# Kernel tuning notes

Measured on AMD Instinct MI355X. Metric: run time of the kernel, lower is better.

The kernel has to match this reference:

```python
import jax, jax.numpy as jnp
import numpy as np

SPATIAL_SHAPES = ((100, 100), (50, 50), (25, 25), (13, 13))
B, C, NH, NL, NP, DFF = 4, 256, 8, 4, 4, 1024
HD = C // NH
L = sum(h * w for h, w in SPATIAL_SHAPES)  # 13294


def _xavier(key, shape):
    s = (6.0 / (shape[0] + shape[1])) ** 0.5
    return jax.random.uniform(key, shape, jnp.float32, -s, s)


def setup_inputs():
    key = jax.random.key(0)
    ks = jax.random.split(key, 12)
    ss = jnp.array(SPATIAL_SHAPES, jnp.int32)
    lsi = jnp.concatenate([jnp.zeros((1,), jnp.int32), jnp.cumsum(ss[:, 0] * ss[:, 1])[:-1].astype(jnp.int32)])
    return {
        "query": jax.random.normal(ks[0], (B, L, C), jnp.float32),
        "query_pos": jax.random.normal(ks[1], (B, L, C), jnp.float32),
        "reference_points": jax.random.uniform(ks[2], (B, L, NL, 2), jnp.float32),
        "spatial_shapes": ss,
        "level_start_index": lsi,
        "v_W": _xavier(ks[3], (C, C)), "v_b": jnp.zeros((C,), jnp.float32),
        "off_W": 0.01 * jax.random.normal(ks[4], (C, NH * NL * NP * 2), jnp.float32),
        "off_b": 0.1 * jax.random.normal(ks[5], (NH * NL * NP * 2,), jnp.float32),
        "aw_W": 0.01 * jax.random.normal(ks[6], (C, NH * NL * NP), jnp.float32),
        "aw_b": jnp.zeros((NH * NL * NP,), jnp.float32),
        "out_W": _xavier(ks[7], (C, C)), "out_b": jnp.zeros((C,), jnp.float32),
        "ln1_g": jnp.ones((C,), jnp.float32), "ln1_b": jnp.zeros((C,), jnp.float32),
        "lin1_W": _xavier(ks[8], (C, DFF)), "lin1_b": jnp.zeros((DFF,), jnp.float32),
        "lin2_W": _xavier(ks[9], (DFF, C)), "lin2_b": jnp.zeros((C,), jnp.float32),
        "ln2_g": jnp.ones((C,), jnp.float32), "ln2_b": jnp.zeros((C,), jnp.float32),
    }


def _layer_norm(x, g, b):
    mu = x.mean(-1, keepdims=True)
    var = ((x - mu) ** 2).mean(-1, keepdims=True)
    return (x - mu) * jax.lax.rsqrt(var + 1e-5) * g + b


def _msda(q, value, reference_points, v_W, v_b, off_W, off_b, aw_W, aw_b, out_W, out_b):
    # value projection, split heads -> [B, NH, L, HD]
    v = (value @ v_W + v_b).reshape(B, L, NH, HD).transpose(0, 2, 1, 3)
    off = (q @ off_W + off_b).reshape(B, L, NH, NL, NP, 2)
    aw = jax.nn.softmax((q @ aw_W + aw_b).reshape(B, L, NH, NL * NP), axis=-1)
    aw = aw.reshape(B, L, NH, NL, NP).transpose(0, 2, 1, 3, 4)  # [B,NH,L,NL,NP]
    # offset normalizer is (W, H) per level, matching (x, y) coords
    norm = jnp.array([[w, h] for h, w in SPATIAL_SHAPES], q.dtype)
    loc = reference_points[:, :, None, :, None, :] + off / norm[None, None, None, :, None, :]
    loc = loc.transpose(0, 2, 1, 3, 4, 5)  # [B,NH,L,NL,NP,2]
    acc = jnp.zeros((B, NH, L, HD), q.dtype)
    start = 0
    for l, (H_, W_) in enumerate(SPATIAL_SHAPES):
        v_l = jax.lax.dynamic_slice_in_dim(v, start, H_ * W_, axis=2)  # [B,NH,HW,HD]
        # grid_sample(align_corners=False): pixel = loc*size - 0.5
        x = loc[:, :, :, l, :, 0] * W_ - 0.5  # [B,NH,L,NP]
        y = loc[:, :, :, l, :, 1] * H_ - 0.5
        x0 = jnp.floor(x); y0 = jnp.floor(y)
        lx = x - x0; ly = y - y0
        x0i = x0.astype(jnp.int32); y0i = y0.astype(jnp.int32)

        def corner(yi, xi, w):
            valid = (yi >= 0) & (yi < H_) & (xi >= 0) & (xi < W_)  # zero padding
            idx = jnp.clip(yi, 0, H_ - 1) * W_ + jnp.clip(xi, 0, W_ - 1)
            g = jnp.take_along_axis(v_l, idx.reshape(B, NH, L * NP, 1), axis=2)
            g = g.reshape(B, NH, L, NP, HD)
            return g * (w * valid)[..., None]

        s = (corner(y0i, x0i, (1 - ly) * (1 - lx))
             + corner(y0i, x0i + 1, (1 - ly) * lx)
             + corner(y0i + 1, x0i, ly * (1 - lx))
             + corner(y0i + 1, x0i + 1, ly * lx))  # [B,NH,L,NP,HD]
        acc = acc + (s * aw[:, :, :, l, :, None]).sum(3)
        start += H_ * W_
    out = acc.transpose(0, 2, 1, 3).reshape(B, L, C)
    return out @ out_W + out_b


def _forward(query, query_pos, reference_points, v_W, v_b, off_W, off_b, aw_W, aw_b,
             out_W, out_b, ln1_g, ln1_b, lin1_W, lin1_b, lin2_W, lin2_b, ln2_g, ln2_b):
    q = query + query_pos
    src2 = _msda(q, query, reference_points, v_W, v_b, off_W, off_b, aw_W, aw_b, out_W, out_b)
    x = _layer_norm(query + src2, ln1_g, ln1_b)
    ffn = jax.nn.relu(x @ lin1_W + lin1_b) @ lin2_W + lin2_b
    return _layer_norm(x + ffn, ln2_g, ln2_b)


def reference(query, query_pos, reference_points, spatial_shapes, level_start_index,
              v_W, v_b, off_W, off_b, aw_W, aw_b, out_W, out_b,
              ln1_g, ln1_b, lin1_W, lin1_b, lin2_W, lin2_b, ln2_g, ln2_b):
    # spatial_shapes / level_start_index are consistent with the static SPATIAL_SHAPES
    # constant (shapes must be static for reshapes under jit).
    return _forward(query, query_pos, reference_points, v_W, v_b, off_W, off_b, aw_W, aw_b,
                    out_W, out_b, ln1_g, ln1_b, lin1_W, lin1_b, lin2_W, lin2_b, ln2_g, ln2_b)
```

## Files before the change

### kernel.cpp

```cpp
#include <hip/hip_runtime.h>
#include <hip/hip_bf16.h>
#include <cstddef>

constexpr int Ll   = 13294;
constexpr int NROW = 4 * Ll;
constexpr int MP   = 53248;

typedef __bf16       bf8v __attribute__((ext_vector_type(8)));
typedef float        f4v  __attribute__((ext_vector_type(4)));
typedef unsigned int u4v  __attribute__((ext_vector_type(4)));

template<bool RELU, bool OUTF, bool OUTB>
__global__ __launch_bounds__(256)
void gemm_mfma(const __hip_bfloat16* __restrict__ A, const __hip_bfloat16* __restrict__ Bt,
               const float* __restrict__ bias, const float* __restrict__ bias2,
               float* __restrict__ Cf, __hip_bfloat16* __restrict__ Cb,
               int M, int N, int K)
{
    __shared__ __hip_bfloat16 As[128 * 32];
    __shared__ __hip_bfloat16 Bs[128 * 32];
    const int tid  = threadIdx.x;
    const int wid  = tid >> 6;
    const int lane = tid & 63;
    const int m0 = blockIdx.y * 128;
    const int n0 = blockIdx.x * 128;
    const int wm = wid >> 1, wn = wid & 1;
    const int fr = lane & 15, fq = lane >> 4;
    const int sr = lane >> 2;
    const int sc = (lane & 3) * 8;

    f4v acc[4][4] = {};

    for (int k0 = 0; k0 < K; k0 += 32) {
        #pragma unroll
        for (int i = 0; i < 2; ++i) {
            const int s = wid * 2 + i;
            const __hip_bfloat16* sa = A  + (size_t)(m0 + s * 16 + sr) * K + k0 + sc;
            const __hip_bfloat16* sb = Bt + (size_t)(n0 + s * 16 + sr) * K + k0 + sc;
            __builtin_amdgcn_global_load_lds(
                (const __attribute__((address_space(1))) void*)sa,
                (__attribute__((address_space(3))) void*)&As[s * 512], 16, 0, 0);
            __builtin_amdgcn_global_load_lds(
                (const __attribute__((address_space(1))) void*)sb,
                (__attribute__((address_space(3))) void*)&Bs[s * 512], 16, 0, 0);
        }
        __syncthreads();

        bf8v a[4], b[4];
        #pragma unroll
        for (int r = 0; r < 4; ++r) {
            a[r] = __builtin_bit_cast(bf8v, *(const u4v*)&As[(wm * 64 + r * 16 + fr) * 32 + fq * 8]);
            b[r] = __builtin_bit_cast(bf8v, *(const u4v*)&Bs[(wn * 64 + r * 16 + fr) * 32 + fq * 8]);
        }
        #pragma unroll
        for (int nr = 0; nr < 4; ++nr)
            #pragma unroll
            for (int mr = 0; mr < 4; ++mr)
                acc[nr][mr] = __builtin_amdgcn_mfma_f32_16x16x32_bf16(b[nr], a[mr], acc[nr][mr], 0, 0, 0);
        __syncthreads();
    }

    #pragma unroll
    for (int nr = 0; nr < 4; ++nr) {
        const int colbase = n0 + wn * 64 + nr * 16 + fq * 4;
        const float* bp = (bias2 != nullptr && colbase >= 256) ? (bias2 - 256) : bias;
        const float4 b4 = *(const float4*)&bp[colbase];
        #pragma unroll
        for (int mr = 0; mr < 4; ++mr) {
            const int row = m0 + wm * 64 + mr * 16 + fr;
            f4v v = acc[nr][mr];
            v[0] += b4.x; v[1] += b4.y; v[2] += b4.z; v[3] += b4.w;
            if (RELU) {
                v[0] = fmaxf(v[0], 0.f); v[1] = fmaxf(v[1], 0.f);
                v[2] = fmaxf(v[2], 0.f); v[3] = fmaxf(v[3], 0.f);
            }
            if (OUTF)
                *(float4*)&Cf[(size_t)row * N + colbase] = make_float4(v[0], v[1], v[2], v[3]);
            if (OUTB) {
                union { ushort4 u; __hip_bfloat16 h[4]; } pk;
                pk.h[0] = __float2bfloat16(v[0]); pk.h[1] = __float2bfloat16(v[1]);
                pk.h[2] = __float2bfloat16(v[2]); pk.h[3] = __float2bfloat16(v[3]);
                *(ushort4*)&Cb[(size_t)row * N + colbase] = pk.u;
            }
        }
    }
}

template<bool STOREB, bool RESB>
__global__ __launch_bounds__(256)
void gemm_ln(const __hip_bfloat16* __restrict__ A, const __hip_bfloat16* __restrict__ Bt,
             const float* __restrict__ bias,
             const float* __restrict__ resF, const __hip_bfloat16* __restrict__ resB,
             int Mres,
             const float* __restrict__ g, const float* __restrict__ be,
             float* __restrict__ outF, int MstoreF,
             __hip_bfloat16* __restrict__ outB,
             int K)
{
    __shared__ __hip_bfloat16 As[64 * 32];
    __shared__ __hip_bfloat16 Bs[256 * 32];
    __shared__ float red[2][64][2];
    const int tid  = threadIdx.x;
    const int wid  = tid >> 6;
    const int lane = tid & 63;
    const int m0 = blockIdx.x * 64;
    const int wm = wid >> 1, wn = wid & 1;
    const int fr = lane & 15, fq = lane >> 4;
    const int sr = lane >> 2;
    const int sc = (lane & 3) * 8;

    f4v acc[8][2] = {};

    for (int k0 = 0; k0 < K; k0 += 32) {
        {
            const __hip_bfloat16* sa = A + (size_t)(m0 + wid * 16 + sr) * K + k0 + sc;
            __builtin_amdgcn_global_load_lds(
                (const __attribute__((address_space(1))) void*)sa,
                (__attribute__((address_space(3))) void*)&As[wid * 512], 16, 0, 0);
        }
        #pragma unroll
        for (int i = 0; i < 4; ++i) {
            const int s = wid * 4 + i;
            const __hip_bfloat16* sb = Bt + (size_t)(s * 16 + sr) * K + k0 + sc;
            __builtin_amdgcn_global_load_lds(
                (const __attribute__((address_space(1))) void*)sb,
                (__attribute__((address_space(3))) void*)&Bs[s * 512], 16, 0, 0);
        }
        __syncthreads();

        bf8v a[2], b[8];
        #pragma unroll
        for (int r = 0; r < 2; ++r)
            a[r] = __builtin_bit_cast(bf8v, *(const u4v*)&As[(wm * 32 + r * 16 + fr) * 32 + fq * 8]);
        #pragma unroll
        for (int r = 0; r < 8; ++r)
            b[r] = __builtin_bit_cast(bf8v, *(const u4v*)&Bs[(wn * 128 + r * 16 + fr) * 32 + fq * 8]);
        #pragma unroll
        for (int nr = 0; nr < 8; ++nr)
            #pragma unroll
            for (int mr = 0; mr < 2; ++mr)
                acc[nr][mr] = __builtin_amdgcn_mfma_f32_16x16x32_bf16(b[nr], a[mr], acc[nr][mr], 0, 0, 0);
        __syncthreads();
    }

    float s2[2] = {}, q2[2] = {};
    #pragma unroll
    for (int nr = 0; nr < 8; ++nr) {
        const int colbase = wn * 128 + nr * 16 + fq * 4;
        const float4 b4 = *(const float4*)&bias[colbase];
        #pragma unroll
        for (int mr = 0; mr < 2; ++mr) {
            const int row = m0 + wm * 32 + mr * 16 + fr;
            f4v x = acc[nr][mr];
            x[0] += b4.x; x[1] += b4.y; x[2] += b4.z; x[3] += b4.w;
            if (RESB) {
                const ushort4 r4 = *(const ushort4*)&resB[(size_t)row * 256 + colbase];
                x[0] += __builtin_bit_cast(float, (unsigned)r4.x << 16);
                x[1] += __builtin_bit_cast(float, (unsigned)r4.y << 16);
                x[2] += __builtin_bit_cast(float, (unsigned)r4.z << 16);
                x[3] += __builtin_bit_cast(float, (unsigned)r4.w << 16);
            } else if (row < Mres) {
                const float4 r4 = *(const float4*)&resF[(size_t)row * 256 + colbase];
                x[0] += r4.x; x[1] += r4.y; x[2] += r4.z; x[3] += r4.w;
            }
            acc[nr][mr] = x;
            s2[mr] += x[0] + x[1] + x[2] + x[3];
            q2[mr] += x[0]*x[0] + x[1]*x[1] + x[2]*x[2] + x[3]*x[3];
        }
    }
    #pragma unroll
    for (int mr = 0; mr < 2; ++mr) {
        s2[mr] += __shfl_xor(s2[mr], 16, 64);
        q2[mr] += __shfl_xor(q2[mr], 16, 64);
        s2[mr] += __shfl_xor(s2[mr], 32, 64);
        q2[mr] += __shfl_xor(q2[mr], 32, 64);
    }
    if (fq == 0) {
        #pragma unroll
        for (int mr = 0; mr < 2; ++mr) {
            red[wn][wm * 32 + mr * 16 + fr][0] = s2[mr];
            red[wn][wm * 32 + mr * 16 + fr][1] = q2[mr];
        }
    }
    __syncthreads();
    float mean[2], rinv[2];
    #pragma unroll
    for (int mr = 0; mr < 2; ++mr) {
        const int r = wm * 32 + mr * 16 + fr;
        const float ss = red[0][r][0] + red[1][r][0];
        const float qq = red[0][r][1] + red[1][r][1];
        mean[mr] = ss * (1.f / 256.f);
        const float var = qq * (1.f / 256.f) - mean[mr] * mean[mr];
        rinv[mr] = rsqrtf(var + 1e-5f);
    }
    #pragma unroll
    for (int nr = 0; nr < 8; ++nr) {
        const int colbase = wn * 128 + nr * 16 + fq * 4;
        const float4 g4 = *(const float4*)&g[colbase];
        const float4 e4 = *(const float4*)&be[colbase];
        #pragma unroll
        for (int mr = 0; mr < 2; ++mr) {
            const int row = m0 + wm * 32 + mr * 16 + fr;
            const f4v x = acc[nr][mr];
            float y0 = (x[0] - mean[mr]) * rinv[mr] * g4.x + e4.x;
            float y1 = (x[1] - mean[mr]) * rinv[mr] * g4.y + e4.y;
            float y2 = (x[2] - mean[mr]) * rinv[mr] * g4.z + e4.z;
            float y3 = (x[3] - mean[mr]) * rinv[mr] * g4.w + e4.w;
            if (row < MstoreF)
                *(float4*)&outF[(size_t)row * 256 + colbase] = make_float4(y0, y1, y2, y3);
            if (STOREB) {
                union { ushort4 u; __hip_bfloat16 h[4]; } pk;
                pk.h[0] = __float2bfloat16(y0); pk.h[1] = __float2bfloat16(y1);
                pk.h[2] = __float2bfloat16(y2); pk.h[3] = __float2bfloat16(y3);
                *(ushort4*)&outB[(size_t)row * 256 + colbase] = pk.u;
            }
        }
    }
}

__global__ __launch_bounds__(256)
void prep_weights(const float* __restrict__ vW, const float* __restrict__ offW,
                  const float* __restrict__ awW, const float* __restrict__ outW,
                  const float* __restrict__ w1, const float* __restrict__ w2,
                  __hip_bfloat16* __restrict__ vWt, __hip_bfloat16* __restrict__ catWt,
                  __hip_bfloat16* __restrict__ outWt, __hip_bfloat16* __restrict__ w1t,
                  __hip_bfloat16* __restrict__ w2t)
{
    int i = blockIdx.x * 256 + threadIdx.x;
    if (i < 65536) { const int n = i >> 8, k = i & 255;
        vWt[i] = __float2bfloat16(vW[(size_t)k * 256 + n]); return; }
    i -= 65536;
    if (i < 98304) { const int n = i >> 8, k = i & 255;
        catWt[i] = __float2bfloat16(n < 256 ? offW[(size_t)k * 256 + n]
                                            : awW[(size_t)k * 128 + n - 256]); return; }
    i -= 98304;
    if (i < 65536) { const int n = i >> 8, k = i & 255;
        outWt[i] = __float2bfloat16(outW[(size_t)k * 256 + n]); return; }
    i -= 65536;
    if (i < 262144) { const int n = i >> 8, k = i & 255;
        w1t[i] = __float2bfloat16(w1[(size_t)k * 1024 + n]); return; }
    i -= 262144;
    { const int n = i >> 10, k = i & 1023;
        w2t[i] = __float2bfloat16(w2[(size_t)k * 256 + n]); }
}

__global__ __launch_bounds__(256)
void cvt_both(const float* __restrict__ q, const float* __restrict__ qp,
              __hip_bfloat16* __restrict__ qb, __hip_bfloat16* __restrict__ qpb)
{
    const int i   = blockIdx.x * 256 + threadIdx.x;
    const int row = i >> 5;
    union { u4v u; __hip_bfloat16 h[8]; } p1, p2;
    if (row >= NROW) {
        u4v z = {0u, 0u, 0u, 0u};
        p1.u = z; p2.u = z;
    } else {
        const size_t e = (size_t)i * 8;
        float4 x0 = *(const float4*)&q[e];
        float4 x1 = *(const float4*)&q[e + 4];
        float4 y0 = *(const float4*)&qp[e];
        float4 y1 = *(const float4*)&qp[e + 4];
        p1.h[0] = __float2bfloat16(x0.x); p1.h[1] = __float2bfloat16(x0.y);
        p1.h[2] = __float2bfloat16(x0.z); p1.h[3] = __float2bfloat16(x0.w);
        p1.h[4] = __float2bfloat16(x1.x); p1.h[5] = __float2bfloat16(x1.y);
        p1.h[6] = __float2bfloat16(x1.z); p1.h[7] = __float2bfloat16(x1.w);
        p2.h[0] = __float2bfloat16(x0.x + y0.x); p2.h[1] = __float2bfloat16(x0.y + y0.y);
        p2.h[2] = __float2bfloat16(x0.z + y0.z); p2.h[3] = __float2bfloat16(x0.w + y0.w);
        p2.h[4] = __float2bfloat16(x1.x + y1.x); p2.h[5] = __float2bfloat16(x1.y + y1.y);
        p2.h[6] = __float2bfloat16(x1.z + y1.z); p2.h[7] = __float2bfloat16(x1.w + y1.w);
    }
    *(u4v*)&qb[(size_t)i * 8]  = p1.u;
    *(u4v*)&qpb[(size_t)i * 8] = p2.u;
}

__device__ __forceinline__ float blo(unsigned u) { return __builtin_bit_cast(float, u << 16); }
__device__ __forceinline__ float bhi(unsigned u) { return __builtin_bit_cast(float, u & 0xffff0000u); }

__global__ __launch_bounds__(256)
void msda_sample3(const __hip_bfloat16* __restrict__ v, const float* __restrict__ cat,
                  const float* __restrict__ refp, __hip_bfloat16* __restrict__ accO)
{
    __shared__ int   sIdx[1024][4];
    __shared__ float sW[1024][4];
    const int row0 = blockIdx.x * 8;
    const int tid  = threadIdx.x;

    #pragma unroll
    for (int it = 0; it < 4; ++it) {
        const int item = it * 256 + tid;
        const int p = item & 15, h = (item >> 4) & 7, r = item >> 7;
        const int row = row0 + r;
        const int lvl = p >> 2;
        const float logit = cat[(size_t)row * 384 + 256 + h * 16 + p];
        float mx = logit;
        #pragma unroll
        for (int o = 1; o < 16; o <<= 1) mx = fmaxf(mx, __shfl_xor(mx, o, 64));
        const float e = __expf(logit - mx);
        float s = e;
        #pragma unroll
        for (int o = 1; o < 16; o <<= 1) s += __shfl_xor(s, o, 64);
        const float aw = e / s;

        const int Hs[4] = {100, 50, 25, 13};
        const int Ss[4] = {0, 10000, 12500, 13125};
        const int   Wl = Hs[lvl];
        const float Wf = (float)Wl;
        const float ox = cat[(size_t)row * 384 + h * 32 + p * 2 + 0];
        const float oy = cat[(size_t)row * 384 + h * 32 + p * 2 + 1];
        const float rx = refp[(size_t)row * 8 + lvl * 2 + 0];
        const float ry = refp[(size_t)row * 8 + lvl * 2 + 1];
        const float x = (rx + ox / Wf) * Wf - 0.5f;
        const float y = (ry + oy / Wf) * Wf - 0.5f;
        const float x0f = floorf(x), y0f = floorf(y);
        const float lx = x - x0f, ly = y - y0f;
        const int x0 = (int)x0f, y0 = (int)y0f;
        const int b = row / Ll;
        const int vbase = b * Ll + Ss[lvl];
        int ixr[4]; float wr[4];
        #pragma unroll
        for (int c = 0; c < 4; ++c) {
            const int cy = c >> 1, cx = c & 1;
            const int yi = y0 + cy, xi = x0 + cx;
            const bool ok = (yi >= 0) & (yi < Wl) & (xi >= 0) & (xi < Wl);
            const int yc = min(max(yi, 0), Wl - 1);
            const int xc = min(max(xi, 0), Wl - 1);
            const float wt = (cy ? ly : 1.f - ly) * (cx ? lx : 1.f - lx);
            ixr[c] = (vbase + yc * Wl + xc) * 512;
            wr[c]  = ok ? aw * wt : 0.f;
        }
        const int item2 = (item & ~15) | ((item & 15) ^ h);
        *(int4*)&sIdx[item2][0] = make_int4(ixr[0], ixr[1], ixr[2], ixr[3]);
        *(float4*)&sW[item2][0] = make_float4(wr[0], wr[1], wr[2], wr[3]);
    }
    __syncthreads();

    const int r   = tid >> 5;
    const int h   = (tid >> 2) & 7;
    const int oct = tid & 3;
    const int row = row0 + r;
    const char* vB = (const char*)v + (h * 32 + oct * 8) * 2;
    const int ibase = r * 128 + h * 16;
    float acc[8] = {};
    #pragma unroll
    for (int i = 0; i < 16; ++i) {
        const int idx = ibase + (i ^ h);
        const int4   ix = *(const int4*)&sIdx[idx][0];
        const float4 wv = *(const float4*)&sW[idx][0];
        u4v u0 = *(const u4v*)(vB + (unsigned)ix.x);
        u4v u1 = *(const u4v*)(vB + (unsigned)ix.y);
        u4v u2 = *(const u4v*)(vB + (unsigned)ix.z);
        u4v u3 = *(const u4v*)(vB + (unsigned)ix.w);
        #pragma unroll
        for (int q = 0; q < 4; ++q) {
            acc[2*q]   = fmaf(wv.x, blo(u0[q]), acc[2*q]);
            acc[2*q+1] = fmaf(wv.x, bhi(u0[q]), acc[2*q+1]);
            acc[2*q]   = fmaf(wv.y, blo(u1[q]), acc[2*q]);
            acc[2*q+1] = fmaf(wv.y, bhi(u1[q]), acc[2*q+1]);
            acc[2*q]   = fmaf(wv.z, blo(u2[q]), acc[2*q]);
            acc[2*q+1] = fmaf(wv.z, bhi(u2[q]), acc[2*q+1]);
            acc[2*q]   = fmaf(wv.w, blo(u3[q]), acc[2*q]);
            acc[2*q+1] = fmaf(wv.w, bhi(u3[q]), acc[2*q+1]);
        }
    }
    union { u4v u; __hip_bfloat16 hh[8]; } pk;
    #pragma unroll
    for (int q = 0; q < 8; ++q) pk.hh[q] = __float2bfloat16(acc[q]);
    *(u4v*)&accO[(size_t)row * 256 + h * 32 + oct * 8] = pk.u;
}

extern "C" void kernel_launch(void* const* d_in, const int* in_sizes, int n_in,
                              void* d_out, int out_size, void* d_ws, size_t ws_size,
                              hipStream_t stream)
{
    (void)in_sizes; (void)n_in; (void)out_size; (void)ws_size;
    const float* query = (const float*)d_in[0];
    const float* qpos  = (const float*)d_in[1];
    const float* refp  = (const float*)d_in[2];
    const float* v_W   = (const float*)d_in[5];
    const float* v_b   = (const float*)d_in[6];
    const float* off_W = (const float*)d_in[7];
    const float* off_b = (const float*)d_in[8];
    const float* aw_W  = (const float*)d_in[9];
    const float* aw_b  = (const float*)d_in[10];
    const float* out_W = (const float*)d_in[11];
    const float* out_b = (const float*)d_in[12];
    const float* ln1g  = (const float*)d_in[13];
    const float* ln1b  = (const float*)d_in[14];
    const float* w1    = (const float*)d_in[15];
    const float* b1    = (const float*)d_in[16];
    const float* w2    = (const float*)d_in[17];
    const float* b2    = (const float*)d_in[18];
    const float* ln2g  = (const float*)d_in[19];
    const float* ln2b  = (const float*)d_in[20];
    float* out = (float*)d_out;

    char* ws = (char*)d_ws;
    constexpr size_t CATF_B = (size_t)MP * 384 * 4;
    constexpr size_t HALF_B = (size_t)MP * 256 * 2;
    float*          catf = (float*)ws;
    __hip_bfloat16* qb   = (__hip_bfloat16*)(ws + CATF_B);
    __hip_bfloat16* qpb  = (__hip_bfloat16*)(ws + CATF_B + HALF_B);
    __hip_bfloat16* vbuf = (__hip_bfloat16*)(ws + CATF_B + 2 * HALF_B);
    __hip_bfloat16* accb = qb;
    __hip_bfloat16* xb   = vbuf;
    __hip_bfloat16* hbuf = (__hip_bfloat16*)ws;
    char* wsw = ws + CATF_B + 3 * HALF_B;
    __hip_bfloat16* vWt   = (__hip_bfloat16*)(wsw);
    __hip_bfloat16* catWt = (__hip_bfloat16*)(wsw + 131072);
    __hip_bfloat16* outWt = (__hip_bfloat16*)(wsw + 327680);
    __hip_bfloat16* w1t   = (__hip_bfloat16*)(wsw + 458752);
    __hip_bfloat16* w2t   = (__hip_bfloat16*)(wsw + 983040);

    dim3 blk(256);

    prep_weights<<<2944, blk, 0, stream>>>(v_W, off_W, aw_W, out_W, w1, w2,
                                           vWt, catWt, outWt, w1t, w2t);
    cvt_both<<<MP / 8, blk, 0, stream>>>(query, qpos, qb, qpb);

    gemm_mfma<false, false, true><<<dim3(2, MP / 128), blk, 0, stream>>>(
        qb, vWt, v_b, nullptr, nullptr, vbuf, MP, 256, 256);
    gemm_mfma<false, true, false><<<dim3(3, MP / 128), blk, 0, stream>>>(
        qpb, catWt, off_b, aw_b, catf, nullptr, MP, 384, 256);

    msda_sample3<<<NROW / 8, blk, 0, stream>>>(vbuf, catf, refp, accb);

    gemm_ln<true, false><<<MP / 64, blk, 0, stream>>>(
        accb, outWt, out_b, query, nullptr, NROW, ln1g, ln1b,
        nullptr, 0, xb, 256);

    gemm_mfma<true, false, true><<<dim3(8, MP / 128), blk, 0, stream>>>(
        xb, w1t, b1, nullptr, nullptr, hbuf, MP, 1024, 256);

    gemm_ln<false, true><<<MP / 64, blk, 0, stream>>>(
        hbuf, w2t, b2, nullptr, xb, MP, ln2g, ln2b,
        out, NROW, nullptr, 1024);
}
```

Before: 364.2 us.

## Use bf16 dot2 in MSDA sampling and remap GEMM blocks across XCDs

The sampling kernel now stores its bilinear-times-attention weights as packed bf16 pairs in shared memory and accumulates with v_dot2_f32_bf16 on byte-permuted value pairs, which halves the weight LDS footprint and FMA count. Separately, the MFMA GEMM remaps flat block IDs so consecutive tiles land on the same XCD, aiming for better L2 reuse. Rounding the weights to bf16 adds precision loss, and the remap assumes the block count divides evenly by 8.

```diff
diff --git a/kernel.cpp b/kernel.cpp
--- a/kernel.cpp
+++ b/kernel.cpp
@@ -7,8 +7,27 @@
 constexpr int MP   = 53248;
 
 typedef __bf16       bf8v __attribute__((ext_vector_type(8)));
+typedef __bf16       bf2v __attribute__((ext_vector_type(2)));
 typedef float        f4v  __attribute__((ext_vector_type(4)));
 typedef unsigned int u4v  __attribute__((ext_vector_type(4)));
+
+#if defined(__has_builtin)
+#  if __has_builtin(__builtin_amdgcn_fdot2_f32_bf16)
+#    define HAVE_DOT2_BF16 1
+#  endif
+#endif
+#ifndef HAVE_DOT2_BF16
+#  define HAVE_DOT2_BF16 0
+#endif
+
+__device__ __forceinline__ void xcd_remap(int& m0, int& n0)
+{
+    const int nwg  = gridDim.x * gridDim.y;
+    const int flat = blockIdx.y * gridDim.x + blockIdx.x;
+    const int w    = (flat & 7) * (nwg >> 3) + (flat >> 3);
+    n0 = (w % gridDim.x) * 128;
+    m0 = (w / gridDim.x) * 128;
+}
 
 template<bool RELU, bool OUTF, bool OUTB>
 __global__ __launch_bounds__(256)
@@ -22,8 +41,8 @@
     const int tid  = threadIdx.x;
     const int wid  = tid >> 6;
     const int lane = tid & 63;
-    const int m0 = blockIdx.y * 128;
-    const int n0 = blockIdx.x * 128;
+    int m0, n0;
+    xcd_remap(m0, n0);
     const int wm = wid >> 1, wn = wid & 1;
     const int fr = lane & 15, fq = lane >> 4;
     const int sr = lane >> 2;
@@ -277,11 +296,11 @@
 __device__ __forceinline__ float bhi(unsigned u) { return __builtin_bit_cast(float, u & 0xffff0000u); }
 
 __global__ __launch_bounds__(256)
-void msda_sample3(const __hip_bfloat16* __restrict__ v, const float* __restrict__ cat,
+void msda_sample4(const __hip_bfloat16* __restrict__ v, const float* __restrict__ cat,
                   const float* __restrict__ refp, __hip_bfloat16* __restrict__ accO)
 {
-    __shared__ int   sIdx[1024][4];
-    __shared__ float sW[1024][4];
+    __shared__ int      sIdx[1024][4];
+    __shared__ unsigned sWpk[1024][2];
     const int row0 = blockIdx.x * 8;
     const int tid  = threadIdx.x;
 
@@ -301,9 +320,9 @@
         for (int o = 1; o < 16; o <<= 1) s += __shfl_xor(s, o, 64);
         const float aw = e / s;
 
-        const int Hs[4] = {100, 50, 25, 13};
-        const int Ss[4] = {0, 10000, 12500, 13125};
-        const int   Wl = Hs[lvl];
+        const int Hs_[4] = {100, 50, 25, 13};
+        const int Ss[4]  = {0, 10000, 12500, 13125};
+        const int   Wl = Hs_[lvl];
         const float Wf = (float)Wl;
         const float ox = cat[(size_t)row * 384 + h * 32 + p * 2 + 0];
         const float oy = cat[(size_t)row * 384 + h * 32 + p * 2 + 1];
@@ -316,7 +335,7 @@
         const int x0 = (int)x0f, y0 = (int)y0f;
         const int b = row / Ll;
         const int vbase = b * Ll + Ss[lvl];
-        int ixr[4]; float wr[4];
+        int ixr[4]; unsigned short wb[4];
         #pragma unroll
         for (int c = 0; c < 4; ++c) {
             const int cy = c >> 1, cx = c & 1;
@@ -326,11 +345,13 @@
             const int xc = min(max(xi, 0), Wl - 1);
             const float wt = (cy ? ly : 1.f - ly) * (cx ? lx : 1.f - lx);
             ixr[c] = (vbase + yc * Wl + xc) * 512;
-            wr[c]  = ok ? aw * wt : 0.f;
+            const __hip_bfloat16 hw = __float2bfloat16(ok ? aw * wt : 0.f);
+            wb[c] = __builtin_bit_cast(unsigned short, hw);
         }
         const int item2 = (item & ~15) | ((item & 15) ^ h);
         *(int4*)&sIdx[item2][0] = make_int4(ixr[0], ixr[1], ixr[2], ixr[3]);
-        *(float4*)&sW[item2][0] = make_float4(wr[0], wr[1], wr[2], wr[3]);
+        sWpk[item2][0] = (unsigned)wb[0] | ((unsigned)wb[1] << 16);
+        sWpk[item2][1] = (unsigned)wb[2] | ((unsigned)wb[3] << 16);
     }
     __syncthreads();
 
@@ -344,23 +365,41 @@
     #pragma unroll
     for (int i = 0; i < 16; ++i) {
         const int idx = ibase + (i ^ h);
-        const int4   ix = *(const int4*)&sIdx[idx][0];
-        const float4 wv = *(const float4*)&sW[idx][0];
+        const int4  ix = *(const int4*)&sIdx[idx][0];
+        const uint2 wp = *(const uint2*)&sWpk[idx][0];
         u4v u0 = *(const u4v*)(vB + (unsigned)ix.x);
         u4v u1 = *(const u4v*)(vB + (unsigned)ix.y);
         u4v u2 = *(const u4v*)(vB + (unsigned)ix.z);
         u4v u3 = *(const u4v*)(vB + (unsigned)ix.w);
+#if HAVE_DOT2_BF16
+        const bf2v w01 = __builtin_bit_cast(bf2v, wp.x);
+        const bf2v w23 = __builtin_bit_cast(bf2v, wp.y);
         #pragma unroll
         for (int q = 0; q < 4; ++q) {
-            acc[2*q]   = fmaf(wv.x, blo(u0[q]), acc[2*q]);
-            acc[2*q+1] = fmaf(wv.x, bhi(u0[q]), acc[2*q+1]);
-            acc[2*q]   = fmaf(wv.y, blo(u1[q]), acc[2*q]);
-            acc[2*q+1] = fmaf(wv.y, bhi(u1[q]), acc[2*q+1]);
-            acc[2*q]   = fmaf(wv.z, blo(u2[q]), acc[2*q]);
-            acc[2*q+1] = fmaf(wv.z, bhi(u2[q]), acc[2*q+1]);
-            acc[2*q]   = fmaf(wv.w, blo(u3[q]), acc[2*q]);
-            acc[2*q+1] = fmaf(wv.w, bhi(u3[q]), acc[2*q+1]);
-        }
+            const unsigned lo01 = __builtin_amdgcn_perm(u1[q], u0[q], 0x05040100u);
+            const unsigned hi01 = __builtin_amdgcn_perm(u1[q], u0[q], 0x07060302u);
+            const unsigned lo23 = __builtin_amdgcn_perm(u3[q], u2[q], 0x05040100u);
+            const unsigned hi23 = __builtin_amdgcn_perm(u3[q], u2[q], 0x07060302u);
+            acc[2*q]   = __builtin_amdgcn_fdot2_f32_bf16(__builtin_bit_cast(bf2v, lo01), w01, acc[2*q],   false);
+            acc[2*q]   = __builtin_amdgcn_fdot2_f32_bf16(__builtin_bit_cast(bf2v, lo23), w23, acc[2*q],   false);
+            acc[2*q+1] = __builtin_amdgcn_fdot2_f32_bf16(__builtin_bit_cast(bf2v, hi01), w01, acc[2*q+1], false);
+            acc[2*q+1] = __builtin_amdgcn_fdot2_f32_bf16(__builtin_bit_cast(bf2v, hi23), w23, acc[2*q+1], false);
+        }
+#else
+        const float w0 = blo(wp.x), w1 = bhi(wp.x);
+        const float w2 = blo(wp.y), w3 = bhi(wp.y);
+        #pragma unroll
+        for (int q = 0; q < 4; ++q) {
+            acc[2*q]   = fmaf(w0, blo(u0[q]), acc[2*q]);
+            acc[2*q+1] = fmaf(w0, bhi(u0[q]), acc[2*q+1]);
+            acc[2*q]   = fmaf(w1, blo(u1[q]), acc[2*q]);
+            acc[2*q+1] = fmaf(w1, bhi(u1[q]), acc[2*q+1]);
+            acc[2*q]   = fmaf(w2, blo(u2[q]), acc[2*q]);
+            acc[2*q+1] = fmaf(w2, bhi(u2[q]), acc[2*q+1]);
+            acc[2*q]   = fmaf(w3, blo(u3[q]), acc[2*q]);
+            acc[2*q+1] = fmaf(w3, bhi(u3[q]), acc[2*q+1]);
+        }
+#endif
     }
     union { u4v u; __hip_bfloat16 hh[8]; } pk;
     #pragma unroll
@@ -422,7 +461,7 @@
     gemm_mfma<false, true, false><<<dim3(3, MP / 128), blk, 0, stream>>>(
         qpb, catWt, off_b, aw_b, catf, nullptr, MP, 384, 256);
 
-    msda_sample3<<<NROW / 8, blk, 0, stream>>>(vbuf, catf, refp, accb);
+    msda_sample4<<<NROW / 8, blk, 0, stream>>>(vbuf, catf, refp, accb);
 
     gemm_ln<true, false><<<MP / 64, blk, 0, stream>>>(
         accb, outWt, out_b, query, nullptr, NROW, ln1g, ln1b,
```

Result: no change. 357.6 us (-1.8%).
